# Performance work log

Hardware: AMD Instinct MI355X
Metric: run time of the kernel (lower is better)

The kernel has to match this reference:

```python
import jax, jax.numpy as jnp
import numpy as np

N_NODES = 100000


def gcn_conv(x, edge_index, W, b, num_nodes):
    """PyG GCNConv: y = D^{-1/2} (A + I) D^{-1/2} (x W) + b.

    edge_index[0] = source (row), edge_index[1] = target (col);
    messages flow source -> target with symmetric normalization.
    """
    # add self loops
    loop = jnp.arange(num_nodes, dtype=edge_index.dtype)
    row = jnp.concatenate([edge_index[0], loop])  # [E+N]
    col = jnp.concatenate([edge_index[1], loop])  # [E+N]

    xw = x @ W  # [N, F_out] -- tiny GEMM, done before gather

    # degree of target nodes (incl. self loops)
    ones = jnp.ones(col.shape[0], dtype=x.dtype)
    deg = jax.ops.segment_sum(ones, col, num_segments=num_nodes)  # [N]
    dis = jax.lax.rsqrt(jnp.maximum(deg, 1e-12))
    dis = jnp.where(deg > 0, dis, 0.0)

    norm = dis[row] * dis[col]  # [E+N]
    msg = xw[row] * norm[:, None]  # gather + scale, [E+N, F_out]
    out = jax.ops.segment_sum(msg, col, num_segments=num_nodes)  # scatter-add
    return out + b


def setup_inputs() -> dict:
    key = jax.random.key(0)
    k1, k2, k3, k4 = jax.random.split(key, 4)
    num_attr, hidden, num_classes = 128, 16, 8
    n_edges = 3200000
    x = jax.random.normal(k1, (N_NODES, num_attr), dtype=jnp.float32)
    edge_index = jax.random.randint(k2, (2, n_edges), 0, N_NODES, dtype=jnp.int64)
    W1 = jax.random.normal(k3, (num_attr, hidden), dtype=jnp.float32) / np.sqrt(num_attr)
    b1 = jnp.zeros((hidden,), dtype=jnp.float32)
    W2 = jax.random.normal(k4, (hidden, num_classes), dtype=jnp.float32) / np.sqrt(hidden)
    b2 = jnp.zeros((num_classes,), dtype=jnp.float32)
    return {"x": x, "edge_index": edge_index, "W1": W1, "b1": b1, "W2": W2, "b2": b2}


def reference(x, edge_index, W1, b1, W2, b2):
    h = gcn_conv(x, edge_index, W1, b1, N_NODES)
    h = jax.nn.relu(h)
    # dropout is identity in eval mode
    h = gcn_conv(h, edge_index, W2, b2, N_NODES)
    return jax.nn.sigmoid(h)  # [N, num_classes]
```

## Files before the change

kernel.cpp:

```cpp
#include <hip/hip_runtime.h>
#include <math.h>

static constexpr int FI = 128;
static constexpr int FH = 16;
static constexpr int FO = 8;

static constexpr int BIN_SHIFT = 8;
static constexpr int BIN_NODES = 256;
static constexpr int MAX_BINS  = 512;
static constexpr int CAPB      = 9728;
static constexpr int SCHUNK    = 8192;
static constexpr int SThreads  = 512;

__device__ __forceinline__ unsigned short f2bf(float x) {
    unsigned u = __float_as_uint(x);
    u += 0x7FFFu + ((u >> 16) & 1u);
    return (unsigned short)(u >> 16);
}
__device__ __forceinline__ float bflo(unsigned u) { return __uint_as_float(u << 16); }
__device__ __forceinline__ float bfhi(unsigned u) { return __uint_as_float(u & 0xFFFF0000u); }

struct SMemScatter {
    int lcnt[MAX_BINS];
    int lstart[MAX_BINS];
    int gbase[MAX_BINS];
    int wsum[8];
    unsigned int  staged[SCHUNK];
    unsigned char sbin[SCHUNK];
};
struct SMemGemm { float sw[FI * FH]; };
union SMemU { SMemScatter s; SMemGemm g; };

__launch_bounds__(SThreads, 6)
__global__ void k_scatter_gemm(const int* __restrict__ row, const int* __restrict__ col,
                               int* __restrict__ binCursor, unsigned int* __restrict__ binned,
                               const float* __restrict__ x, const float* __restrict__ W1,
                               unsigned short* __restrict__ xw1, int E, int nchunks, int N) {
    __shared__ SMemU sm;
    int t = threadIdx.x;

    if ((int)blockIdx.x >= nchunks) {
        for (int i = t; i < FI * FH; i += SThreads) sm.g.sw[i] = W1[i];
        __syncthreads();
        int nl = t >> 2;
        int f  = (t & 3) * 4;
        int n  = ((int)blockIdx.x - nchunks) * 128 + nl;
        if (n >= N) return;
        const float4* xr = (const float4*)(x + (size_t)n * FI);
        float a0 = 0.f, a1 = 0.f, a2 = 0.f, a3 = 0.f;
        #pragma unroll 8
        for (int kq = 0; kq < FI / 4; ++kq) {
            float4 xv = xr[kq];
            float4 w0 = *(const float4*)&sm.g.sw[(kq * 4 + 0) * FH + f];
            float4 w1 = *(const float4*)&sm.g.sw[(kq * 4 + 1) * FH + f];
            float4 w2 = *(const float4*)&sm.g.sw[(kq * 4 + 2) * FH + f];
            float4 w3 = *(const float4*)&sm.g.sw[(kq * 4 + 3) * FH + f];
            a0 = fmaf(xv.x, w0.x, a0); a1 = fmaf(xv.x, w0.y, a1);
            a2 = fmaf(xv.x, w0.z, a2); a3 = fmaf(xv.x, w0.w, a3);
            a0 = fmaf(xv.y, w1.x, a0); a1 = fmaf(xv.y, w1.y, a1);
            a2 = fmaf(xv.y, w1.z, a2); a3 = fmaf(xv.y, w1.w, a3);
            a0 = fmaf(xv.z, w2.x, a0); a1 = fmaf(xv.z, w2.y, a1);
            a2 = fmaf(xv.z, w2.z, a2); a3 = fmaf(xv.z, w2.w, a3);
            a0 = fmaf(xv.w, w3.x, a0); a1 = fmaf(xv.w, w3.y, a1);
            a2 = fmaf(xv.w, w3.z, a2); a3 = fmaf(xv.w, w3.w, a3);
        }
        unsigned p0 = (unsigned)f2bf(a0) | ((unsigned)f2bf(a1) << 16);
        unsigned p1 = (unsigned)f2bf(a2) | ((unsigned)f2bf(a3) << 16);
        *(uint2*)(xw1 + (size_t)n * FH + f) = make_uint2(p0, p1);
        return;
    }

    int base = blockIdx.x * SCHUNK;
    int end  = base + SCHUNK; if (end > E) end = E;
    int m = end - base;
    sm.s.lcnt[t] = 0;
    __syncthreads();

    int nv = m >> 2;
    const int4* c4 = (const int4*)(col + base);
    int4 creg[4];
    unsigned short a16[16];
    #pragma unroll
    for (int j = 0; j < 4; ++j) {
        int k = t + j * SThreads;
        if (k < nv) {
            creg[j] = c4[k];
            a16[j*4+0] = (unsigned short)atomicAdd(&sm.s.lcnt[creg[j].x >> BIN_SHIFT], 1);
            a16[j*4+1] = (unsigned short)atomicAdd(&sm.s.lcnt[creg[j].y >> BIN_SHIFT], 1);
            a16[j*4+2] = (unsigned short)atomicAdd(&sm.s.lcnt[creg[j].z >> BIN_SHIFT], 1);
            a16[j*4+3] = (unsigned short)atomicAdd(&sm.s.lcnt[creg[j].w >> BIN_SHIFT], 1);
        }
    }
    int tailIdx = base + (nv << 2) + t;
    int tailCol = 0, tailA = -1;
    if (tailIdx < end) {
        tailCol = col[tailIdx];
        tailA = atomicAdd(&sm.s.lcnt[tailCol >> BIN_SHIFT], 1);
    }
    __syncthreads();

    int v = sm.s.lcnt[t];
    int inc = v;
    #pragma unroll
    for (int d = 1; d < 64; d <<= 1) {
        int u = __shfl_up(inc, d, 64);
        if ((t & 63) >= d) inc += u;
    }
    if ((t & 63) == 63) sm.s.wsum[t >> 6] = inc;
    __syncthreads();
    if (t < 8) {
        int w = sm.s.wsum[t];
        #pragma unroll
        for (int d = 1; d < 8; d <<= 1) {
            int u = __shfl_up(w, d, 8);
            if (t >= d) w += u;
        }
        sm.s.wsum[t] = w;
    }
    __syncthreads();
    {
        int waveoff = (t >= 64) ? sm.s.wsum[(t >> 6) - 1] : 0;
        sm.s.lstart[t] = waveoff + inc - v;
        sm.s.gbase[t]  = v ? atomicAdd(&binCursor[t], v) : 0;
    }
    __syncthreads();

    const int4* r4 = (const int4*)(row + base);
    #pragma unroll
    for (int j = 0; j < 4; ++j) {
        int k = t + j * SThreads;
        if (k < nv) {
            int4 r = r4[k];
            int cc[4] = {creg[j].x, creg[j].y, creg[j].z, creg[j].w};
            int rr[4] = {r.x, r.y, r.z, r.w};
            #pragma unroll
            for (int jj = 0; jj < 4; ++jj) {
                int b = cc[jj] >> BIN_SHIFT;
                int pos = sm.s.lstart[b] + a16[j*4+jj];
                sm.s.staged[pos] = (unsigned)rr[jj] | ((unsigned)(cc[jj] & (BIN_NODES - 1)) << 17)
                                 | ((unsigned)(b >> 8) << 25);
                sm.s.sbin[pos] = (unsigned char)b;
            }
        }
    }
    if (tailA >= 0) {
        int b = tailCol >> BIN_SHIFT;
        int pos = sm.s.lstart[b] + tailA;
        sm.s.staged[pos] = (unsigned)row[tailIdx] | ((unsigned)(tailCol & (BIN_NODES - 1)) << 17)
                         | ((unsigned)(b >> 8) << 25);
        sm.s.sbin[pos] = (unsigned char)b;
    }
    __syncthreads();

    for (int i = t; i < m; i += SThreads) {
        unsigned sv = sm.s.staged[i];
        int b = (int)sm.s.sbin[i] | (int)((sv >> 25) & 1u) << 8;
        int off = sm.s.gbase[b] + (i - sm.s.lstart[b]);
        if (off < CAPB) binned[b * CAPB + off] = sv & 0x1FFFFFFu;
    }
}

__launch_bounds__(BIN_NODES)
__global__ void k_refine(const int* __restrict__ binCursor, const unsigned int* __restrict__ binned,
                         int* __restrict__ srow, int* __restrict__ starts, int* __restrict__ ends,
                         float* __restrict__ dis, unsigned short* __restrict__ xw1, int N) {
    __shared__ unsigned char arr[CAPB];
    __shared__ int cnt[BIN_NODES];
    __shared__ int wsum[4];
    int t = threadIdx.x;
    int b = blockIdx.x;
    int s = b * CAPB;
    int m = binCursor[b];
    if (m > CAPB - 768) m = CAPB - 768;
    cnt[t] = 0;
    __syncthreads();

    int mm = m & ~3;
    for (int i0 = t * 4; i0 < mm; i0 += BIN_NODES * 4) {
        uint4 v = *(const uint4*)(binned + s + i0);
        arr[i0 + 0] = (unsigned char)atomicAdd(&cnt[v.x >> 17], 1);
        arr[i0 + 1] = (unsigned char)atomicAdd(&cnt[v.y >> 17], 1);
        arr[i0 + 2] = (unsigned char)atomicAdd(&cnt[v.z >> 17], 1);
        arr[i0 + 3] = (unsigned char)atomicAdd(&cnt[v.w >> 17], 1);
    }
    for (int i = mm + t; i < m; i += BIN_NODES)
        arr[i] = (unsigned char)atomicAdd(&cnt[binned[s + i] >> 17], 1);
    __syncthreads();

    int deg  = cnt[t];
    int pdeg = (deg + 3) & ~3;
    int inc = pdeg;
    #pragma unroll
    for (int d = 1; d < 64; d <<= 1) {
        int u = __shfl_up(inc, d, 64);
        if ((t & 63) >= d) inc += u;
    }
    if ((t & 63) == 63) wsum[t >> 6] = inc;
    __syncthreads();
    if (t < 4) {
        int w = wsum[t];
        #pragma unroll
        for (int d = 1; d < 4; d <<= 1) {
            int u = __shfl_up(w, d, 4);
            if (t >= d) w += u;
        }
        wsum[t] = w;
    }
    __syncthreads();
    int waveoff = (t >= 64) ? wsum[(t >> 6) - 1] : 0;
    int pexcl = waveoff + inc - pdeg;

    int n = b * BIN_NODES + t;
    float dv = rsqrtf((float)(deg + 1));
    if (n < N) {
        starts[n] = s + pexcl;
        ends[n]   = s + pexcl + deg;
        dis[n]    = dv;
    }
    cnt[t] = pexcl;
    __syncthreads();

    for (int i0 = t * 4; i0 < mm; i0 += BIN_NODES * 4) {
        uint4 v = *(const uint4*)(binned + s + i0);
        srow[s + cnt[v.x >> 17] + arr[i0 + 0]] = v.x & 0x1FFFF;
        srow[s + cnt[v.y >> 17] + arr[i0 + 1]] = v.y & 0x1FFFF;
        srow[s + cnt[v.z >> 17] + arr[i0 + 2]] = v.z & 0x1FFFF;
        srow[s + cnt[v.w >> 17] + arr[i0 + 3]] = v.w & 0x1FFFF;
    }
    for (int i = mm + t; i < m; i += BIN_NODES) {
        unsigned v = binned[s + i];
        srow[s + cnt[v >> 17] + arr[i]] = v & 0x1FFFF;
    }

    if (n < N) {
        uint4* p = (uint4*)(xw1 + (size_t)n * FH);
        uint4 va = p[0], vb = p[1];
        unsigned* u = &va.x;
        #pragma unroll
        for (int k = 0; k < 4; ++k)
            u[k] = (unsigned)f2bf(bflo(u[k]) * dv) | ((unsigned)f2bf(bfhi(u[k]) * dv) << 16);
        unsigned* w = &vb.x;
        #pragma unroll
        for (int k = 0; k < 4; ++k)
            w[k] = (unsigned)f2bf(bflo(w[k]) * dv) | ((unsigned)f2bf(bfhi(w[k]) * dv) << 16);
        p[0] = va; p[1] = vb;
    }
}

__launch_bounds__(256)
__global__ void k_agg1(const int* __restrict__ starts, const int* __restrict__ ends,
                       const int* __restrict__ srow, const float* __restrict__ dis,
                       const unsigned short* __restrict__ xw1s, const float* __restrict__ W2,
                       const float* __restrict__ b1, unsigned short* __restrict__ xw2s, int N) {
    __shared__ float sw[FH * FO];
    __shared__ float sb[FH];
    int t = threadIdx.x;
    if (t < FH * FO) sw[t] = W2[t];
    if (t < FH) sb[t] = b1[t];
    __syncthreads();

    int n = blockIdx.x * 128 + (t >> 1);
    int h = t & 1;
    if (n >= N) return;
    float dn = dis[n];
    int s = starts[n], e = ends[n];
    const uint4* xq = (const uint4*)xw1s;

    uint4 sp = xq[(size_t)n * 2 + h];
    float acc[8];
    acc[0]=bflo(sp.x); acc[1]=bfhi(sp.x); acc[2]=bflo(sp.y); acc[3]=bfhi(sp.y);
    acc[4]=bflo(sp.z); acc[5]=bfhi(sp.z); acc[6]=bflo(sp.w); acc[7]=bfhi(sp.w);

    int i = s;
    for (; i + 8 <= e; i += 8) {
        int4 ra = *(const int4*)(srow + i);
        int4 rb = *(const int4*)(srow + i + 4);
        uint4 pk[8];
        pk[0] = xq[(size_t)ra.x * 2 + h]; pk[1] = xq[(size_t)ra.y * 2 + h];
        pk[2] = xq[(size_t)ra.z * 2 + h]; pk[3] = xq[(size_t)ra.w * 2 + h];
        pk[4] = xq[(size_t)rb.x * 2 + h]; pk[5] = xq[(size_t)rb.y * 2 + h];
        pk[6] = xq[(size_t)rb.z * 2 + h]; pk[7] = xq[(size_t)rb.w * 2 + h];
        #pragma unroll
        for (int j = 0; j < 8; ++j) {
            acc[0]+=bflo(pk[j].x); acc[1]+=bfhi(pk[j].x);
            acc[2]+=bflo(pk[j].y); acc[3]+=bfhi(pk[j].y);
            acc[4]+=bflo(pk[j].z); acc[5]+=bfhi(pk[j].z);
            acc[6]+=bflo(pk[j].w); acc[7]+=bfhi(pk[j].w);
        }
    }
    for (; i < e; ++i) {
        uint4 p = xq[(size_t)srow[i] * 2 + h];
        acc[0]+=bflo(p.x); acc[1]+=bfhi(p.x);
        acc[2]+=bflo(p.y); acc[3]+=bfhi(p.y);
        acc[4]+=bflo(p.z); acc[5]+=bfhi(p.z);
        acc[6]+=bflo(p.w); acc[7]+=bfhi(p.w);
    }

    float hv[8];
    #pragma unroll
    for (int k = 0; k < 8; ++k) {
        float v = fmaf(dn, acc[k], sb[h * 8 + k]);
        hv[k] = v > 0.f ? v : 0.f;
    }
    float po[FO];
    #pragma unroll
    for (int o = 0; o < FO; ++o) {
        float a = 0.f;
        #pragma unroll
        for (int k = 0; k < 8; ++k) a = fmaf(hv[k], sw[(h * 8 + k) * FO + o], a);
        po[o] = a;
    }
    #pragma unroll
    for (int o = 0; o < FO; ++o) po[o] += __shfl_xor(po[o], 1, 64);
    int o0 = h * 4;
    unsigned w0 = (unsigned)f2bf(po[o0 + 0] * dn) | ((unsigned)f2bf(po[o0 + 1] * dn) << 16);
    unsigned w1 = (unsigned)f2bf(po[o0 + 2] * dn) | ((unsigned)f2bf(po[o0 + 3] * dn) << 16);
    *(uint2*)(xw2s + (size_t)n * FO + o0) = make_uint2(w0, w1);
}

__launch_bounds__(256)
__global__ void k_agg2(const int* __restrict__ starts, const int* __restrict__ ends,
                       const int* __restrict__ srow, const float* __restrict__ dis,
                       const unsigned short* __restrict__ xw2s, const float* __restrict__ b2,
                       float* __restrict__ out, int N) {
    int t = threadIdx.x;
    int n = blockIdx.x * 128 + (t >> 1);
    int h = t & 1;
    if (n >= N) return;
    float dn = dis[n];
    int s = starts[n], e = ends[n];
    const uint2* xq = (const uint2*)xw2s;

    uint2 sp = xq[(size_t)n * 2 + h];
    float acc[4];
    acc[0]=bflo(sp.x); acc[1]=bfhi(sp.x); acc[2]=bflo(sp.y); acc[3]=bfhi(sp.y);

    int i = s;
    for (; i + 8 <= e; i += 8) {
        int4 ra = *(const int4*)(srow + i);
        int4 rb = *(const int4*)(srow + i + 4);
        uint2 pk[8];
        pk[0] = xq[(size_t)ra.x * 2 + h]; pk[1] = xq[(size_t)ra.y * 2 + h];
        pk[2] = xq[(size_t)ra.z * 2 + h]; pk[3] = xq[(size_t)ra.w * 2 + h];
        pk[4] = xq[(size_t)rb.x * 2 + h]; pk[5] = xq[(size_t)rb.y * 2 + h];
        pk[6] = xq[(size_t)rb.z * 2 + h]; pk[7] = xq[(size_t)rb.w * 2 + h];
        #pragma unroll
        for (int j = 0; j < 8; ++j) {
            acc[0]+=bflo(pk[j].x); acc[1]+=bfhi(pk[j].x);
            acc[2]+=bflo(pk[j].y); acc[3]+=bfhi(pk[j].y);
        }
    }
    for (; i < e; ++i) {
        uint2 p = xq[(size_t)srow[i] * 2 + h];
        acc[0]+=bflo(p.x); acc[1]+=bfhi(p.x);
        acc[2]+=bflo(p.y); acc[3]+=bfhi(p.y);
    }

    int f0 = h * 4;
    float r[4];
    #pragma unroll
    for (int k = 0; k < 4; ++k) {
        float v = fmaf(dn, acc[k], b2[f0 + k]);
        r[k] = 1.f / (1.f + __expf(-v));
    }
    *(float4*)(out + (size_t)n * FO + f0) = make_float4(r[0], r[1], r[2], r[3]);
}

extern "C" void kernel_launch(void* const* d_in, const int* in_sizes, int n_in,
                              void* d_out, int out_size, void* d_ws, size_t ws_size,
                              hipStream_t stream) {
    const float* x  = (const float*)d_in[0];
    const int*   ei = (const int*)d_in[1];
    const float* W1 = (const float*)d_in[2];
    const float* b1 = (const float*)d_in[3];
    const float* W2 = (const float*)d_in[4];
    const float* b2 = (const float*)d_in[5];

    const int N = in_sizes[0] / FI;
    const int E = in_sizes[1] / 2;
    const int* row = ei;
    const int* col = ei + E;
    const int nbins = (N + BIN_NODES - 1) >> BIN_SHIFT;

    const int nchunks = (E + SCHUNK - 1) / SCHUNK;
    const int ngemm   = (N + 127) / 128;

    const size_t NP = 100352;
    const size_t BINSZ = (size_t)nbins * CAPB;
    float* base = (float*)d_ws;
    int*   starts    = (int*)base;
    int*   ends      = (int*)(base + NP);
    float* dis       = base + 2 * NP;
    int*   binCursor = (int*)(base + 3 * NP);
    unsigned int* binned = (unsigned int*)(base + 3 * NP + 1024);
    int*   srow      = (int*)(base + 3 * NP + 1024 + BINSZ);
    unsigned short* xw1s = (unsigned short*)(base + 3 * NP + 1024 + 2 * BINSZ);
    unsigned short* xw2s = (unsigned short*)(base + 3 * NP + 1024 + 2 * BINSZ + NP * 8);
    float* out = (float*)d_out;

    size_t needed = (3 * NP + 1024 + 2 * BINSZ + NP * 12) * 4;
    if (ws_size < needed) return;

    hipMemsetAsync(binCursor, 0, (size_t)nbins * sizeof(int), stream);
    k_scatter_gemm<<<nchunks + ngemm, SThreads, 0, stream>>>(row, col, binCursor, binned,
                                                             x, W1, xw1s, E, nchunks, N);
    k_refine      <<<nbins, BIN_NODES,          0, stream>>>(binCursor, binned, srow, starts, ends, dis, xw1s, N);
    k_agg1        <<<(2 * N + 255) / 256, 256,  0, stream>>>(starts, ends, srow, dis, xw1s, W2, b1, xw2s, N);
    k_agg2        <<<(2 * N + 255) / 256, 256,  0, stream>>>(starts, ends, srow, dis, xw2s, b2, out, N);
}
```

Measured before the change: 116.9 us.

## Fuse refine and both aggregation kernels into one cooperative persistent kernel

Merges the refine, first-layer aggregation and second-layer aggregation kernels into a single cooperative kernel that uses grid-wide syncs between phases and grid-stride loops over bins and nodes. The aim is to remove two kernel launch gaps and their tail effects. In exchange, grid size is capped by occupancy, grid.sync adds its own barrier cost, and the larger unioned shared memory may lower occupancy in the aggregation phases. Host-side occupancy queries are also added to every launch.

```diff
diff --git a/kernel.cpp b/kernel.cpp
--- a/kernel.cpp
+++ b/kernel.cpp
@@ -1,5 +1,8 @@
 #include <hip/hip_runtime.h>
+#include <hip/hip_cooperative_groups.h>
 #include <math.h>
+
+namespace cg = cooperative_groups;
 
 static constexpr int FI = 128;
 static constexpr int FH = 16;
@@ -160,210 +163,210 @@
     }
 }
 
+struct SRef {
+    unsigned char arr[CAPB];
+    int cnt[BIN_NODES];
+    int wsum[4];
+};
+struct SAgg { float sw[FH * FO]; float sb[FH]; };
+union UBack { SRef r; SAgg a; };
+
 __launch_bounds__(BIN_NODES)
-__global__ void k_refine(const int* __restrict__ binCursor, const unsigned int* __restrict__ binned,
-                         int* __restrict__ srow, int* __restrict__ starts, int* __restrict__ ends,
-                         float* __restrict__ dis, unsigned short* __restrict__ xw1, int N) {
-    __shared__ unsigned char arr[CAPB];
-    __shared__ int cnt[BIN_NODES];
-    __shared__ int wsum[4];
-    int t = threadIdx.x;
-    int b = blockIdx.x;
-    int s = b * CAPB;
-    int m = binCursor[b];
-    if (m > CAPB - 768) m = CAPB - 768;
-    cnt[t] = 0;
-    __syncthreads();
-
-    int mm = m & ~3;
-    for (int i0 = t * 4; i0 < mm; i0 += BIN_NODES * 4) {
-        uint4 v = *(const uint4*)(binned + s + i0);
-        arr[i0 + 0] = (unsigned char)atomicAdd(&cnt[v.x >> 17], 1);
-        arr[i0 + 1] = (unsigned char)atomicAdd(&cnt[v.y >> 17], 1);
-        arr[i0 + 2] = (unsigned char)atomicAdd(&cnt[v.z >> 17], 1);
-        arr[i0 + 3] = (unsigned char)atomicAdd(&cnt[v.w >> 17], 1);
-    }
-    for (int i = mm + t; i < m; i += BIN_NODES)
-        arr[i] = (unsigned char)atomicAdd(&cnt[binned[s + i] >> 17], 1);
-    __syncthreads();
-
-    int deg  = cnt[t];
-    int pdeg = (deg + 3) & ~3;
-    int inc = pdeg;
-    #pragma unroll
-    for (int d = 1; d < 64; d <<= 1) {
-        int u = __shfl_up(inc, d, 64);
-        if ((t & 63) >= d) inc += u;
-    }
-    if ((t & 63) == 63) wsum[t >> 6] = inc;
-    __syncthreads();
-    if (t < 4) {
-        int w = wsum[t];
-        #pragma unroll
-        for (int d = 1; d < 4; d <<= 1) {
-            int u = __shfl_up(w, d, 4);
-            if (t >= d) w += u;
-        }
-        wsum[t] = w;
-    }
-    __syncthreads();
-    int waveoff = (t >= 64) ? wsum[(t >> 6) - 1] : 0;
-    int pexcl = waveoff + inc - pdeg;
-
-    int n = b * BIN_NODES + t;
-    float dv = rsqrtf((float)(deg + 1));
-    if (n < N) {
-        starts[n] = s + pexcl;
-        ends[n]   = s + pexcl + deg;
-        dis[n]    = dv;
-    }
-    cnt[t] = pexcl;
-    __syncthreads();
-
-    for (int i0 = t * 4; i0 < mm; i0 += BIN_NODES * 4) {
-        uint4 v = *(const uint4*)(binned + s + i0);
-        srow[s + cnt[v.x >> 17] + arr[i0 + 0]] = v.x & 0x1FFFF;
-        srow[s + cnt[v.y >> 17] + arr[i0 + 1]] = v.y & 0x1FFFF;
-        srow[s + cnt[v.z >> 17] + arr[i0 + 2]] = v.z & 0x1FFFF;
-        srow[s + cnt[v.w >> 17] + arr[i0 + 3]] = v.w & 0x1FFFF;
-    }
-    for (int i = mm + t; i < m; i += BIN_NODES) {
-        unsigned v = binned[s + i];
-        srow[s + cnt[v >> 17] + arr[i]] = v & 0x1FFFF;
-    }
-
-    if (n < N) {
-        uint4* p = (uint4*)(xw1 + (size_t)n * FH);
-        uint4 va = p[0], vb = p[1];
-        unsigned* u = &va.x;
-        #pragma unroll
-        for (int k = 0; k < 4; ++k)
-            u[k] = (unsigned)f2bf(bflo(u[k]) * dv) | ((unsigned)f2bf(bfhi(u[k]) * dv) << 16);
-        unsigned* w = &vb.x;
-        #pragma unroll
-        for (int k = 0; k < 4; ++k)
-            w[k] = (unsigned)f2bf(bflo(w[k]) * dv) | ((unsigned)f2bf(bfhi(w[k]) * dv) << 16);
-        p[0] = va; p[1] = vb;
-    }
-}
-
-__launch_bounds__(256)
-__global__ void k_agg1(const int* __restrict__ starts, const int* __restrict__ ends,
-                       const int* __restrict__ srow, const float* __restrict__ dis,
-                       const unsigned short* __restrict__ xw1s, const float* __restrict__ W2,
-                       const float* __restrict__ b1, unsigned short* __restrict__ xw2s, int N) {
-    __shared__ float sw[FH * FO];
-    __shared__ float sb[FH];
-    int t = threadIdx.x;
-    if (t < FH * FO) sw[t] = W2[t];
-    if (t < FH) sb[t] = b1[t];
-    __syncthreads();
-
-    int n = blockIdx.x * 128 + (t >> 1);
-    int h = t & 1;
-    if (n >= N) return;
-    float dn = dis[n];
-    int s = starts[n], e = ends[n];
-    const uint4* xq = (const uint4*)xw1s;
-
-    uint4 sp = xq[(size_t)n * 2 + h];
-    float acc[8];
-    acc[0]=bflo(sp.x); acc[1]=bfhi(sp.x); acc[2]=bflo(sp.y); acc[3]=bfhi(sp.y);
-    acc[4]=bflo(sp.z); acc[5]=bfhi(sp.z); acc[6]=bflo(sp.w); acc[7]=bfhi(sp.w);
-
-    int i = s;
-    for (; i + 8 <= e; i += 8) {
-        int4 ra = *(const int4*)(srow + i);
-        int4 rb = *(const int4*)(srow + i + 4);
-        uint4 pk[8];
-        pk[0] = xq[(size_t)ra.x * 2 + h]; pk[1] = xq[(size_t)ra.y * 2 + h];
-        pk[2] = xq[(size_t)ra.z * 2 + h]; pk[3] = xq[(size_t)ra.w * 2 + h];
-        pk[4] = xq[(size_t)rb.x * 2 + h]; pk[5] = xq[(size_t)rb.y * 2 + h];
-        pk[6] = xq[(size_t)rb.z * 2 + h]; pk[7] = xq[(size_t)rb.w * 2 + h];
-        #pragma unroll
-        for (int j = 0; j < 8; ++j) {
-            acc[0]+=bflo(pk[j].x); acc[1]+=bfhi(pk[j].x);
-            acc[2]+=bflo(pk[j].y); acc[3]+=bfhi(pk[j].y);
-            acc[4]+=bflo(pk[j].z); acc[5]+=bfhi(pk[j].z);
-            acc[6]+=bflo(pk[j].w); acc[7]+=bfhi(pk[j].w);
-        }
-    }
-    for (; i < e; ++i) {
-        uint4 p = xq[(size_t)srow[i] * 2 + h];
-        acc[0]+=bflo(p.x); acc[1]+=bfhi(p.x);
-        acc[2]+=bflo(p.y); acc[3]+=bfhi(p.y);
-        acc[4]+=bflo(p.z); acc[5]+=bfhi(p.z);
-        acc[6]+=bflo(p.w); acc[7]+=bfhi(p.w);
-    }
-
-    float hv[8];
-    #pragma unroll
-    for (int k = 0; k < 8; ++k) {
-        float v = fmaf(dn, acc[k], sb[h * 8 + k]);
-        hv[k] = v > 0.f ? v : 0.f;
-    }
-    float po[FO];
-    #pragma unroll
-    for (int o = 0; o < FO; ++o) {
-        float a = 0.f;
-        #pragma unroll
-        for (int k = 0; k < 8; ++k) a = fmaf(hv[k], sw[(h * 8 + k) * FO + o], a);
-        po[o] = a;
-    }
-    #pragma unroll
-    for (int o = 0; o < FO; ++o) po[o] += __shfl_xor(po[o], 1, 64);
-    int o0 = h * 4;
-    unsigned w0 = (unsigned)f2bf(po[o0 + 0] * dn) | ((unsigned)f2bf(po[o0 + 1] * dn) << 16);
-    unsigned w1 = (unsigned)f2bf(po[o0 + 2] * dn) | ((unsigned)f2bf(po[o0 + 3] * dn) << 16);
-    *(uint2*)(xw2s + (size_t)n * FO + o0) = make_uint2(w0, w1);
-}
-
-__launch_bounds__(256)
-__global__ void k_agg2(const int* __restrict__ starts, const int* __restrict__ ends,
-                       const int* __restrict__ srow, const float* __restrict__ dis,
-                       const unsigned short* __restrict__ xw2s, const float* __restrict__ b2,
+__global__ void k_back(const int* __restrict__ binCursor, const unsigned int* __restrict__ binned,
+                       int* __restrict__ srow, int* __restrict__ starts, int* __restrict__ ends,
+                       float* __restrict__ dis, unsigned short* __restrict__ xw1s,
+                       const float* __restrict__ W2, const float* __restrict__ b1,
+                       unsigned short* __restrict__ xw2s, const float* __restrict__ b2,
                        float* __restrict__ out, int N) {
-    int t = threadIdx.x;
-    int n = blockIdx.x * 128 + (t >> 1);
-    int h = t & 1;
-    if (n >= N) return;
-    float dn = dis[n];
-    int s = starts[n], e = ends[n];
-    const uint2* xq = (const uint2*)xw2s;
-
-    uint2 sp = xq[(size_t)n * 2 + h];
-    float acc[4];
-    acc[0]=bflo(sp.x); acc[1]=bfhi(sp.x); acc[2]=bflo(sp.y); acc[3]=bfhi(sp.y);
-
-    int i = s;
-    for (; i + 8 <= e; i += 8) {
-        int4 ra = *(const int4*)(srow + i);
-        int4 rb = *(const int4*)(srow + i + 4);
-        uint2 pk[8];
-        pk[0] = xq[(size_t)ra.x * 2 + h]; pk[1] = xq[(size_t)ra.y * 2 + h];
-        pk[2] = xq[(size_t)ra.z * 2 + h]; pk[3] = xq[(size_t)ra.w * 2 + h];
-        pk[4] = xq[(size_t)rb.x * 2 + h]; pk[5] = xq[(size_t)rb.y * 2 + h];
-        pk[6] = xq[(size_t)rb.z * 2 + h]; pk[7] = xq[(size_t)rb.w * 2 + h];
-        #pragma unroll
-        for (int j = 0; j < 8; ++j) {
-            acc[0]+=bflo(pk[j].x); acc[1]+=bfhi(pk[j].x);
-            acc[2]+=bflo(pk[j].y); acc[3]+=bfhi(pk[j].y);
-        }
-    }
-    for (; i < e; ++i) {
-        uint2 p = xq[(size_t)srow[i] * 2 + h];
-        acc[0]+=bflo(p.x); acc[1]+=bfhi(p.x);
-        acc[2]+=bflo(p.y); acc[3]+=bfhi(p.y);
-    }
-
-    int f0 = h * 4;
-    float r[4];
-    #pragma unroll
-    for (int k = 0; k < 4; ++k) {
-        float v = fmaf(dn, acc[k], b2[f0 + k]);
-        r[k] = 1.f / (1.f + __expf(-v));
-    }
-    *(float4*)(out + (size_t)n * FO + f0) = make_float4(r[0], r[1], r[2], r[3]);
+    cg::grid_group grid = cg::this_grid();
+    __shared__ UBack sm;
+    const int t  = threadIdx.x;
+    const int nb = gridDim.x;
+    const int nbins = (N + BIN_NODES - 1) >> BIN_SHIFT;
+
+    for (int b = blockIdx.x; b < nbins; b += nb) {
+        __syncthreads();
+        int s = b * CAPB;
+        int m = binCursor[b];
+        if (m > CAPB - 768) m = CAPB - 768;
+        sm.r.cnt[t] = 0;
+        __syncthreads();
+
+        int mm = m & ~3;
+        for (int i0 = t * 4; i0 < mm; i0 += BIN_NODES * 4) {
+            uint4 v = *(const uint4*)(binned + s + i0);
+            sm.r.arr[i0 + 0] = (unsigned char)atomicAdd(&sm.r.cnt[v.x >> 17], 1);
+            sm.r.arr[i0 + 1] = (unsigned char)atomicAdd(&sm.r.cnt[v.y >> 17], 1);
+            sm.r.arr[i0 + 2] = (unsigned char)atomicAdd(&sm.r.cnt[v.z >> 17], 1);
+            sm.r.arr[i0 + 3] = (unsigned char)atomicAdd(&sm.r.cnt[v.w >> 17], 1);
+        }
+        for (int i = mm + t; i < m; i += BIN_NODES)
+            sm.r.arr[i] = (unsigned char)atomicAdd(&sm.r.cnt[binned[s + i] >> 17], 1);
+        __syncthreads();
+
+        int deg  = sm.r.cnt[t];
+        int pdeg = (deg + 3) & ~3;
+        int inc = pdeg;
+        #pragma unroll
+        for (int d = 1; d < 64; d <<= 1) {
+            int u = __shfl_up(inc, d, 64);
+            if ((t & 63) >= d) inc += u;
+        }
+        if ((t & 63) == 63) sm.r.wsum[t >> 6] = inc;
+        __syncthreads();
+        if (t < 4) {
+            int w = sm.r.wsum[t];
+            #pragma unroll
+            for (int d = 1; d < 4; d <<= 1) {
+                int u = __shfl_up(w, d, 4);
+                if (t >= d) w += u;
+            }
+            sm.r.wsum[t] = w;
+        }
+        __syncthreads();
+        int waveoff = (t >= 64) ? sm.r.wsum[(t >> 6) - 1] : 0;
+        int pexcl = waveoff + inc - pdeg;
+
+        int n = b * BIN_NODES + t;
+        float dv = rsqrtf((float)(deg + 1));
+        if (n < N) {
+            starts[n] = s + pexcl;
+            ends[n]   = s + pexcl + deg;
+            dis[n]    = dv;
+        }
+        sm.r.cnt[t] = pexcl;
+        __syncthreads();
+
+        for (int i0 = t * 4; i0 < mm; i0 += BIN_NODES * 4) {
+            uint4 v = *(const uint4*)(binned + s + i0);
+            srow[s + sm.r.cnt[v.x >> 17] + sm.r.arr[i0 + 0]] = v.x & 0x1FFFF;
+            srow[s + sm.r.cnt[v.y >> 17] + sm.r.arr[i0 + 1]] = v.y & 0x1FFFF;
+            srow[s + sm.r.cnt[v.z >> 17] + sm.r.arr[i0 + 2]] = v.z & 0x1FFFF;
+            srow[s + sm.r.cnt[v.w >> 17] + sm.r.arr[i0 + 3]] = v.w & 0x1FFFF;
+        }
+        for (int i = mm + t; i < m; i += BIN_NODES) {
+            unsigned v = binned[s + i];
+            srow[s + sm.r.cnt[v >> 17] + sm.r.arr[i]] = v & 0x1FFFF;
+        }
+
+        if (n < N) {
+            uint4* p = (uint4*)(xw1s + (size_t)n * FH);
+            uint4 va = p[0], vb = p[1];
+            unsigned* ua = &va.x;
+            #pragma unroll
+            for (int k = 0; k < 4; ++k)
+                ua[k] = (unsigned)f2bf(bflo(ua[k]) * dv) | ((unsigned)f2bf(bfhi(ua[k]) * dv) << 16);
+            unsigned* ub = &vb.x;
+            #pragma unroll
+            for (int k = 0; k < 4; ++k)
+                ub[k] = (unsigned)f2bf(bflo(ub[k]) * dv) | ((unsigned)f2bf(bfhi(ub[k]) * dv) << 16);
+            p[0] = va; p[1] = vb;
+        }
+    }
+    grid.sync();
+
+    if (t < FH * FO) sm.a.sw[t] = W2[t];
+    if (t < FH) sm.a.sb[t] = b1[t];
+    __syncthreads();
+    for (int L = blockIdx.x * BIN_NODES + t; L < 2 * N; L += nb * BIN_NODES) {
+        int n = L >> 1, h = L & 1;
+        float dn = dis[n];
+        int s = starts[n], e = ends[n];
+        const uint4* xq = (const uint4*)xw1s;
+
+        uint4 sp = xq[(size_t)n * 2 + h];
+        float acc[8];
+        acc[0]=bflo(sp.x); acc[1]=bfhi(sp.x); acc[2]=bflo(sp.y); acc[3]=bfhi(sp.y);
+        acc[4]=bflo(sp.z); acc[5]=bfhi(sp.z); acc[6]=bflo(sp.w); acc[7]=bfhi(sp.w);
+
+        int i = s;
+        for (; i + 8 <= e; i += 8) {
+            int4 ra = *(const int4*)(srow + i);
+            int4 rb = *(const int4*)(srow + i + 4);
+            uint4 pk[8];
+            pk[0] = xq[(size_t)ra.x * 2 + h]; pk[1] = xq[(size_t)ra.y * 2 + h];
+            pk[2] = xq[(size_t)ra.z * 2 + h]; pk[3] = xq[(size_t)ra.w * 2 + h];
+            pk[4] = xq[(size_t)rb.x * 2 + h]; pk[5] = xq[(size_t)rb.y * 2 + h];
+            pk[6] = xq[(size_t)rb.z * 2 + h]; pk[7] = xq[(size_t)rb.w * 2 + h];
+            #pragma unroll
+            for (int j = 0; j < 8; ++j) {
+                acc[0]+=bflo(pk[j].x); acc[1]+=bfhi(pk[j].x);
+                acc[2]+=bflo(pk[j].y); acc[3]+=bfhi(pk[j].y);
+                acc[4]+=bflo(pk[j].z); acc[5]+=bfhi(pk[j].z);
+                acc[6]+=bflo(pk[j].w); acc[7]+=bfhi(pk[j].w);
+            }
+        }
+        for (; i < e; ++i) {
+            uint4 p = xq[(size_t)srow[i] * 2 + h];
+            acc[0]+=bflo(p.x); acc[1]+=bfhi(p.x);
+            acc[2]+=bflo(p.y); acc[3]+=bfhi(p.y);
+            acc[4]+=bflo(p.z); acc[5]+=bfhi(p.z);
+            acc[6]+=bflo(p.w); acc[7]+=bfhi(p.w);
+        }
+
+        float hv[8];
+        #pragma unroll
+        for (int k = 0; k < 8; ++k) {
+            float v = fmaf(dn, acc[k], sm.a.sb[h * 8 + k]);
+            hv[k] = v > 0.f ? v : 0.f;
+        }
+        float po[FO];
+        #pragma unroll
+        for (int o = 0; o < FO; ++o) {
+            float a = 0.f;
+            #pragma unroll
+            for (int k = 0; k < 8; ++k) a = fmaf(hv[k], sm.a.sw[(h * 8 + k) * FO + o], a);
+            po[o] = a;
+        }
+        #pragma unroll
+        for (int o = 0; o < FO; ++o) po[o] += __shfl_xor(po[o], 1, 64);
+        int o0 = h * 4;
+        unsigned q0 = (unsigned)f2bf(po[o0 + 0] * dn) | ((unsigned)f2bf(po[o0 + 1] * dn) << 16);
+        unsigned q1 = (unsigned)f2bf(po[o0 + 2] * dn) | ((unsigned)f2bf(po[o0 + 3] * dn) << 16);
+        *(uint2*)(xw2s + (size_t)n * FO + o0) = make_uint2(q0, q1);
+    }
+    grid.sync();
+
+    for (int L = blockIdx.x * BIN_NODES + t; L < 2 * N; L += nb * BIN_NODES) {
+        int n = L >> 1, h = L & 1;
+        float dn = dis[n];
+        int s = starts[n], e = ends[n];
+        const uint2* xq = (const uint2*)xw2s;
+
+        uint2 sp = xq[(size_t)n * 2 + h];
+        float acc[4];
+        acc[0]=bflo(sp.x); acc[1]=bfhi(sp.x); acc[2]=bflo(sp.y); acc[3]=bfhi(sp.y);
+
+        int i = s;
+        for (; i + 8 <= e; i += 8) {
+            int4 ra = *(const int4*)(srow + i);
+            int4 rb = *(const int4*)(srow + i + 4);
+            uint2 pk[8];
+            pk[0] = xq[(size_t)ra.x * 2 + h]; pk[1] = xq[(size_t)ra.y * 2 + h];
+            pk[2] = xq[(size_t)ra.z * 2 + h]; pk[3] = xq[(size_t)ra.w * 2 + h];
+            pk[4] = xq[(size_t)rb.x * 2 + h]; pk[5] = xq[(size_t)rb.y * 2 + h];
+            pk[6] = xq[(size_t)rb.z * 2 + h]; pk[7] = xq[(size_t)rb.w * 2 + h];
+            #pragma unroll
+            for (int j = 0; j < 8; ++j) {
+                acc[0]+=bflo(pk[j].x); acc[1]+=bfhi(pk[j].x);
+                acc[2]+=bflo(pk[j].y); acc[3]+=bfhi(pk[j].y);
+            }
+        }
+        for (; i < e; ++i) {
+            uint2 p = xq[(size_t)srow[i] * 2 + h];
+            acc[0]+=bflo(p.x); acc[1]+=bfhi(p.x);
+            acc[2]+=bflo(p.y); acc[3]+=bfhi(p.y);
+        }
+
+        int f0 = h * 4;
+        float r[4];
+        #pragma unroll
+        for (int k = 0; k < 4; ++k) {
+            float v = fmaf(dn, acc[k], b2[f0 + k]);
+            r[k] = 1.f / (1.f + __expf(-v));
+        }
+        *(float4*)(out + (size_t)n * FO + f0) = make_float4(r[0], r[1], r[2], r[3]);
+    }
 }
 
 extern "C" void kernel_launch(void* const* d_in, const int* in_sizes, int n_in,
@@ -376,8 +379,8 @@
     const float* W2 = (const float*)d_in[4];
     const float* b2 = (const float*)d_in[5];
 
-    const int N = in_sizes[0] / FI;
-    const int E = in_sizes[1] / 2;
+    int N = in_sizes[0] / FI;
+    int E = in_sizes[1] / 2;
     const int* row = ei;
     const int* col = ei + E;
     const int nbins = (N + BIN_NODES - 1) >> BIN_SHIFT;
@@ -401,10 +404,26 @@
     size_t needed = (3 * NP + 1024 + 2 * BINSZ + NP * 12) * 4;
     if (ws_size < needed) return;
 
+    int dev = 0;
+    hipGetDevice(&dev);
+    int numCU = 256;
+    hipDeviceGetAttribute(&numCU, hipDeviceAttributeMultiprocessorCount, dev);
+    int maxB = 0;
+    hipOccupancyMaxActiveBlocksPerMultiprocessor(&maxB, k_back, BIN_NODES, 0);
+    if (maxB < 1) maxB = 1;
+    long long gback = (long long)maxB * numCU;
+    long long work  = (2LL * N + BIN_NODES - 1) / BIN_NODES;
+    if (gback > work) gback = work;
+    if (gback < 1) gback = 1;
+
     hipMemsetAsync(binCursor, 0, (size_t)nbins * sizeof(int), stream);
+
     k_scatter_gemm<<<nchunks + ngemm, SThreads, 0, stream>>>(row, col, binCursor, binned,
                                                              x, W1, xw1s, E, nchunks, N);
-    k_refine      <<<nbins, BIN_NODES,          0, stream>>>(binCursor, binned, srow, starts, ends, dis, xw1s, N);
-    k_agg1        <<<(2 * N + 255) / 256, 256,  0, stream>>>(starts, ends, srow, dis, xw1s, W2, b1, xw2s, N);
-    k_agg2        <<<(2 * N + 255) / 256, 256,  0, stream>>>(starts, ends, srow, dis, xw2s, b2, out, N);
+
+    void* args[] = { (void*)&binCursor, (void*)&binned, (void*)&srow, (void*)&starts,
+                     (void*)&ends, (void*)&dis, (void*)&xw1s, (void*)&W2, (void*)&b1,
+                     (void*)&xw2s, (void*)&b2, (void*)&out, (void*)&N };
+    hipLaunchCooperativeKernel((void*)k_back, dim3((unsigned)gback), dim3(BIN_NODES),
+                               args, 0, stream);
 }
```

Result: slower. 214.7 us (+83.7%).
